# Performance work log

Measured on AMD Instinct MI355X. Metric: run time of the kernel, lower is better.

## Reference

```python
import jax, jax.numpy as jnp
import numpy as np


def setup_inputs() -> dict:
    key = jax.random.key(0)
    k1, k2, k3 = jax.random.split(key, 3)
    B, S, D_IN, D_OUT = 4, 2048, 4096, 4096
    x = jax.random.normal(k1, (B, S, D_IN), dtype=jnp.float32)
    weight = jax.random.normal(k2, (D_OUT, D_IN), dtype=jnp.float32) * 0.02
    bias = jax.random.normal(k3, (D_OUT,), dtype=jnp.float32) * 0.02
    return {"x": x, "weight": weight, "bias": bias}


def reference(x, weight, bias):
    # Column L1 norms over the output dim (torch.norm(w, p=1, dim=0)) -> [in_features]
    column_norms = jnp.abs(weight).sum(axis=0)
    q = jnp.quantile(column_norms, jnp.array([0.05, 0.95], dtype=column_norms.dtype))
    lower, upper = q[0], q[1]
    # NOTE: mask naming follows the source; 'outlier_columns' is actually the middle band.
    outlier_columns = (column_norms > lower) & (column_norms < upper)  # [in]
    binarized = ~outlier_columns  # columns that get rescaled (mask is inverted in source)

    # Row-wise abs-mean over the 'binarized' columns, detached. Shape [out, 1].
    n_bin = binarized.sum().astype(weight.dtype)
    scale = (jnp.abs(weight) * binarized[None, :]).sum(axis=-1, keepdims=True) / n_bin
    scale = jax.lax.stop_gradient(scale)

    # The STE sign assignment in the source is overwritten by w * scale, so the
    # effective binarized-column value is weight * scale (not sign(weight) * scale).
    w_bin = jnp.where(binarized[None, :], weight * scale, weight)  # [out, in]

    # F.linear(x, w_bin, bias)
    out = jnp.einsum('bsd,od->bso', x, w_bin) + bias
    return out
```

## Files before the change

### kernel.cpp

```cpp
#include <hip/hip_runtime.h>
#include <hip/hip_bf16.h>

typedef unsigned short u16;
typedef __bf16 bf16x8 __attribute__((ext_vector_type(8)));
typedef float f32x4 __attribute__((ext_vector_type(4)));
typedef __attribute__((address_space(1))) void* gp1_t;
typedef __attribute__((address_space(3))) void* lp3_t;

#define D_IN   4096
#define D_OUT  4096
#define M_ROWS 8192

#define OFF_NORMS  0u
#define OFF_QVALS  16384u
#define OFF_NBIN   16400u
#define OFF_MASK   16640u
#define OFF_SCALE  33024u
#define OFF_PART   49408u
#define OFF_XB     573696u
#define OFF_WB     67682560u

static __device__ __forceinline__ u16 f2bf(float f) {
    __hip_bfloat16 h = __float2bfloat16(f);
    u16 u; __builtin_memcpy(&u, &h, 2);
    return u;
}

__global__ void colnorm_partial(const float* __restrict__ W, float* __restrict__ part) {
    const int j  = blockIdx.x * 256 + threadIdx.x;
    const int r0 = blockIdx.y * 128;
    float s = 0.f;
    #pragma unroll 4
    for (int r = 0; r < 128; ++r) s += fabsf(W[(size_t)(r0 + r) * D_IN + j]);
    part[blockIdx.y * D_IN + j] = s;
}

__global__ void colnorm_reduce(const float* __restrict__ part, float* __restrict__ norms) {
    const int j = blockIdx.x * 256 + threadIdx.x;
    float s = 0.f;
    #pragma unroll
    for (int p = 0; p < 32; ++p) s += part[p * D_IN + j];
    norms[j] = s;
}

__global__ void rank_select(const float* __restrict__ norms, float* __restrict__ qvals) {
    __shared__ float sn[D_IN];
    const int tid = threadIdx.x;
    for (int i = tid; i < D_IN; i += 256) sn[i] = norms[i];
    __syncthreads();
    const int j = blockIdx.x * 256 + tid;
    const float vj = sn[j];
    int r = 0;
    #pragma unroll 8
    for (int i = 0; i < D_IN; ++i) {
        const float vi = sn[i];
        r += (vi < vj) || (vi == vj && i < j);
    }
    if      (r == 204)  qvals[0] = vj;
    else if (r == 205)  qvals[1] = vj;
    else if (r == 3890) qvals[2] = vj;
    else if (r == 3891) qvals[3] = vj;
}

__global__ void mask_count(const float* __restrict__ norms, const float* __restrict__ qvals,
                           float* __restrict__ mask, float* __restrict__ nbin) {
    __shared__ float wsum[16];
    const int tid = threadIdx.x;
    const float lower = qvals[0] + 0.75f * (qvals[1] - qvals[0]);
    const float upper = qvals[2] + 0.25f * (qvals[3] - qvals[2]);
    int cnt = 0;
    for (int i = tid; i < D_IN; i += 1024) {
        const float v = norms[i];
        const bool bin = !(v > lower && v < upper);
        mask[i] = bin ? 1.0f : 0.0f;
        cnt += bin ? 1 : 0;
    }
    #pragma unroll
    for (int off = 32; off > 0; off >>= 1) cnt += __shfl_down(cnt, off, 64);
    if ((tid & 63) == 0) wsum[tid >> 6] = (float)cnt;
    __syncthreads();
    if (tid == 0) {
        float s = 0.f;
        #pragma unroll
        for (int w = 0; w < 16; ++w) s += wsum[w];
        *nbin = s;
    }
}

__global__ void row_scale(const float* __restrict__ W, const float* __restrict__ mask,
                          const float* __restrict__ nbin, float* __restrict__ scale) {
    const int wave = threadIdx.x >> 6, lane = threadIdx.x & 63;
    const int o = blockIdx.x * 4 + wave;
    const float* row = W + (size_t)o * D_IN;
    float s = 0.f;
    #pragma unroll 4
    for (int j = lane; j < D_IN; j += 64) s += fabsf(row[j]) * mask[j];
    #pragma unroll
    for (int off = 32; off > 0; off >>= 1) s += __shfl_down(s, off, 64);
    if (lane == 0) scale[o] = s / *nbin;
}

__global__ void build_wbin(const float* __restrict__ W, const float* __restrict__ mask,
                           const float* __restrict__ scale, u16* __restrict__ wb) {
    const int o = blockIdx.x;
    const float sc = scale[o];
    const float4* row = (const float4*)(W + (size_t)o * D_IN);
    const float4* m4  = (const float4*)mask;
    ushort4* out = (ushort4*)(wb + (size_t)o * D_IN);
    #pragma unroll
    for (int it = 0; it < 4; ++it) {
        const int c = it * 256 + threadIdx.x;
        const float4 w = row[c];
        const float4 mm = m4[c];
        ushort4 r;
        r.x = f2bf(mm.x != 0.f ? w.x * sc : w.x);
        r.y = f2bf(mm.y != 0.f ? w.y * sc : w.y);
        r.z = f2bf(mm.z != 0.f ? w.z * sc : w.z);
        r.w = f2bf(mm.w != 0.f ? w.w * sc : w.w);
        out[c] = r;
    }
}

__global__ void cast_x(const float* __restrict__ x, u16* __restrict__ xb) {
    const size_t i4 = (size_t)blockIdx.x * 256 + threadIdx.x;
    const float4 v = ((const float4*)x)[i4];
    ushort4 r;
    r.x = f2bf(v.x); r.y = f2bf(v.y); r.z = f2bf(v.z); r.w = f2bf(v.w);
    ((ushort4*)xb)[i4] = r;
}

__global__ __launch_bounds__(256) void gemm_bt(const u16* __restrict__ A, const u16* __restrict__ B,
                                               const float* __restrict__ bias, float* __restrict__ C) {
    __shared__ u16 lA[128 * 32];
    __shared__ u16 lB[128 * 32];
    const int tid  = threadIdx.x;
    const int wave = tid >> 6, lane = tid & 63;
    const int wr = wave >> 1, wc = wave & 1;
    const int m0 = blockIdx.y * 128, n0 = blockIdx.x * 128;

    const int srow = tid >> 2;
    const int scol = (tid & 3) * 8;
    const u16* gA0 = A + (size_t)(m0 + srow) * D_IN + scol;
    const u16* gA1 = A + (size_t)(m0 + 64 + srow) * D_IN + scol;
    const u16* gB0 = B + (size_t)(n0 + srow) * D_IN + scol;
    const u16* gB1 = B + (size_t)(n0 + 64 + srow) * D_IN + scol;
    lp3_t lA0 = (lp3_t)(lA + wave * 512);
    lp3_t lA1 = (lp3_t)(lA + 2048 + wave * 512);
    lp3_t lB0 = (lp3_t)(lB + wave * 512);
    lp3_t lB1 = (lp3_t)(lB + 2048 + wave * 512);

    f32x4 acc[4][4] = {};

    const int koff = (lane >> 4) * 8;
    const int rsel = lane & 15;

    for (int kt = 0; kt < D_IN; kt += 32) {
        __builtin_amdgcn_global_load_lds((gp1_t)(gA0 + kt), lA0, 16, 0, 0);
        __builtin_amdgcn_global_load_lds((gp1_t)(gA1 + kt), lA1, 16, 0, 0);
        __builtin_amdgcn_global_load_lds((gp1_t)(gB0 + kt), lB0, 16, 0, 0);
        __builtin_amdgcn_global_load_lds((gp1_t)(gB1 + kt), lB1, 16, 0, 0);
        __syncthreads();

        bf16x8 af[4], bfv[4];
        #pragma unroll
        for (int mi = 0; mi < 4; ++mi)
            af[mi] = *(const bf16x8*)(lA + (wr * 64 + mi * 16 + rsel) * 32 + koff);
        #pragma unroll
        for (int ni = 0; ni < 4; ++ni)
            bfv[ni] = *(const bf16x8*)(lB + (wc * 64 + ni * 16 + rsel) * 32 + koff);
        #pragma unroll
        for (int mi = 0; mi < 4; ++mi)
            #pragma unroll
            for (int ni = 0; ni < 4; ++ni)
                acc[mi][ni] = __builtin_amdgcn_mfma_f32_16x16x32_bf16(af[mi], bfv[ni], acc[mi][ni], 0, 0, 0);
        __syncthreads();
    }

    const int cm = (lane >> 4) * 4;
    const int cn = lane & 15;
    #pragma unroll
    for (int ni = 0; ni < 4; ++ni) {
        const int n = n0 + wc * 64 + ni * 16 + cn;
        const float bv = bias[n];
        #pragma unroll
        for (int mi = 0; mi < 4; ++mi) {
            const int mbase = m0 + wr * 64 + mi * 16 + cm;
            #pragma unroll
            for (int r = 0; r < 4; ++r)
                C[(size_t)(mbase + r) * D_OUT + n] = acc[mi][ni][r] + bv;
        }
    }
}

extern "C" void kernel_launch(void* const* d_in, const int* in_sizes, int n_in,
                              void* d_out, int out_size, void* d_ws, size_t ws_size,
                              hipStream_t stream) {
    const float* x    = (const float*)d_in[0];
    const float* W    = (const float*)d_in[1];
    const float* bias = (const float*)d_in[2];
    float* out = (float*)d_out;

    char* ws = (char*)d_ws;
    float* norms = (float*)(ws + OFF_NORMS);
    float* qvals = (float*)(ws + OFF_QVALS);
    float* nbin  = (float*)(ws + OFF_NBIN);
    float* mask  = (float*)(ws + OFF_MASK);
    float* scale = (float*)(ws + OFF_SCALE);
    float* part  = (float*)(ws + OFF_PART);
    u16*   xb    = (u16*)(ws + OFF_XB);
    u16*   wb    = (u16*)(ws + OFF_WB);

    colnorm_partial<<<dim3(16, 32), 256, 0, stream>>>(W, part);
    colnorm_reduce<<<16, 256, 0, stream>>>(part, norms);
    rank_select<<<16, 256, 0, stream>>>(norms, qvals);
    mask_count<<<1, 1024, 0, stream>>>(norms, qvals, mask, nbin);
    row_scale<<<1024, 256, 0, stream>>>(W, mask, nbin, scale);
    build_wbin<<<4096, 256, 0, stream>>>(W, mask, scale, wb);
    cast_x<<<32768, 256, 0, stream>>>(x, xb);
    gemm_bt<<<dim3(D_OUT / 128, M_ROWS / 128), 256, 0, stream>>>(xb, wb, bias, out);
}
```

Measured before the change: 703.6 us.

## Fuse preprocessing kernels and swizzle GEMM LDS layout to avoid bank conflicts

Merges the column-norm partial/reduce kernels with the x-to-bf16 cast into one launch, using atomics into a zeroed norms buffer. Also merges mask/count, row-scale and weight-binarize into a single per-row kernel that keeps the row in registers. Separately, it XOR-rotates the 16-byte chunk placement in the GEMM's LDS tiles to cut bank conflicts on fragment reads. The atomic float accumulation makes the column norms order-nondeterministic, which could shift quantile ties slightly.

```diff
diff --git a/kernel.cpp b/kernel.cpp
--- a/kernel.cpp
+++ b/kernel.cpp
@@ -13,10 +13,6 @@
 
 #define OFF_NORMS  0u
 #define OFF_QVALS  16384u
-#define OFF_NBIN   16400u
-#define OFF_MASK   16640u
-#define OFF_SCALE  33024u
-#define OFF_PART   49408u
 #define OFF_XB     573696u
 #define OFF_WB     67682560u
 
@@ -26,21 +22,25 @@
     return u;
 }
 
-__global__ void colnorm_partial(const float* __restrict__ W, float* __restrict__ part) {
-    const int j  = blockIdx.x * 256 + threadIdx.x;
-    const int r0 = blockIdx.y * 128;
-    float s = 0.f;
-    #pragma unroll 4
-    for (int r = 0; r < 128; ++r) s += fabsf(W[(size_t)(r0 + r) * D_IN + j]);
-    part[blockIdx.y * D_IN + j] = s;
-}
-
-__global__ void colnorm_reduce(const float* __restrict__ part, float* __restrict__ norms) {
-    const int j = blockIdx.x * 256 + threadIdx.x;
-    float s = 0.f;
-    #pragma unroll
-    for (int p = 0; p < 32; ++p) s += part[p * D_IN + j];
-    norms[j] = s;
+__global__ __launch_bounds__(256) void k1_cast_colnorm(const float* __restrict__ x,
+                                                       const float* __restrict__ W,
+                                                       u16* __restrict__ xb,
+                                                       float* __restrict__ norms) {
+    const int b = blockIdx.x;
+    if (b < 512) {
+        const int j  = (b & 15) * 256 + threadIdx.x;
+        const int r0 = (b >> 4) * 128;
+        float s = 0.f;
+        #pragma unroll 4
+        for (int r = 0; r < 128; ++r) s += fabsf(W[(size_t)(r0 + r) * D_IN + j]);
+        atomicAdd(&norms[j], s);
+    } else {
+        const size_t i4 = (size_t)(b - 512) * 256 + threadIdx.x;
+        const float4 v = ((const float4*)x)[i4];
+        ushort4 r;
+        r.x = f2bf(v.x); r.y = f2bf(v.y); r.z = f2bf(v.z); r.w = f2bf(v.w);
+        ((ushort4*)xb)[i4] = r;
+    }
 }
 
 __global__ void rank_select(const float* __restrict__ norms, float* __restrict__ qvals) {
@@ -62,71 +62,58 @@
     else if (r == 3891) qvals[3] = vj;
 }
 
-__global__ void mask_count(const float* __restrict__ norms, const float* __restrict__ qvals,
-                           float* __restrict__ mask, float* __restrict__ nbin) {
-    __shared__ float wsum[16];
-    const int tid = threadIdx.x;
+__global__ __launch_bounds__(256) void k3_scale_wbin(const float* __restrict__ W,
+                                                     const float* __restrict__ norms,
+                                                     const float* __restrict__ qvals,
+                                                     u16* __restrict__ wb) {
+    __shared__ float red[8];
+    const int o = blockIdx.x, t = threadIdx.x;
+    const int wave = t >> 6, lane = t & 63;
     const float lower = qvals[0] + 0.75f * (qvals[1] - qvals[0]);
     const float upper = qvals[2] + 0.25f * (qvals[3] - qvals[2]);
-    int cnt = 0;
-    for (int i = tid; i < D_IN; i += 1024) {
-        const float v = norms[i];
-        const bool bin = !(v > lower && v < upper);
-        mask[i] = bin ? 1.0f : 0.0f;
-        cnt += bin ? 1 : 0;
-    }
-    #pragma unroll
-    for (int off = 32; off > 0; off >>= 1) cnt += __shfl_down(cnt, off, 64);
-    if ((tid & 63) == 0) wsum[tid >> 6] = (float)cnt;
+    const float4* row4 = (const float4*)(W + (size_t)o * D_IN);
+    const float4* n4   = (const float4*)norms;
+
+    float4 wv[4];
+    int binbits[4];
+    float cnt = 0.f, sum = 0.f;
+    #pragma unroll
+    for (int it = 0; it < 4; ++it) {
+        const int c = it * 256 + t;
+        wv[it] = row4[c];
+        const float4 nv = n4[c];
+        const bool b0 = !(nv.x > lower && nv.x < upper);
+        const bool b1 = !(nv.y > lower && nv.y < upper);
+        const bool b2 = !(nv.z > lower && nv.z < upper);
+        const bool b3 = !(nv.w > lower && nv.w < upper);
+        binbits[it] = (b0 ? 1 : 0) | (b1 ? 2 : 0) | (b2 ? 4 : 0) | (b3 ? 8 : 0);
+        cnt += (float)(b0 + b1 + b2 + b3);
+        sum += (b0 ? fabsf(wv[it].x) : 0.f) + (b1 ? fabsf(wv[it].y) : 0.f)
+             + (b2 ? fabsf(wv[it].z) : 0.f) + (b3 ? fabsf(wv[it].w) : 0.f);
+    }
+    #pragma unroll
+    for (int off = 32; off > 0; off >>= 1) {
+        cnt += __shfl_down(cnt, off, 64);
+        sum += __shfl_down(sum, off, 64);
+    }
+    if (lane == 0) { red[wave] = cnt; red[4 + wave] = sum; }
     __syncthreads();
-    if (tid == 0) {
-        float s = 0.f;
-        #pragma unroll
-        for (int w = 0; w < 16; ++w) s += wsum[w];
-        *nbin = s;
-    }
-}
-
-__global__ void row_scale(const float* __restrict__ W, const float* __restrict__ mask,
-                          const float* __restrict__ nbin, float* __restrict__ scale) {
-    const int wave = threadIdx.x >> 6, lane = threadIdx.x & 63;
-    const int o = blockIdx.x * 4 + wave;
-    const float* row = W + (size_t)o * D_IN;
-    float s = 0.f;
-    #pragma unroll 4
-    for (int j = lane; j < D_IN; j += 64) s += fabsf(row[j]) * mask[j];
-    #pragma unroll
-    for (int off = 32; off > 0; off >>= 1) s += __shfl_down(s, off, 64);
-    if (lane == 0) scale[o] = s / *nbin;
-}
-
-__global__ void build_wbin(const float* __restrict__ W, const float* __restrict__ mask,
-                           const float* __restrict__ scale, u16* __restrict__ wb) {
-    const int o = blockIdx.x;
-    const float sc = scale[o];
-    const float4* row = (const float4*)(W + (size_t)o * D_IN);
-    const float4* m4  = (const float4*)mask;
+    const float nbin = red[0] + red[1] + red[2] + red[3];
+    const float ssum = red[4] + red[5] + red[6] + red[7];
+    const float sc = ssum / nbin;
+
     ushort4* out = (ushort4*)(wb + (size_t)o * D_IN);
     #pragma unroll
     for (int it = 0; it < 4; ++it) {
-        const int c = it * 256 + threadIdx.x;
-        const float4 w = row[c];
-        const float4 mm = m4[c];
+        const int c = it * 256 + t;
+        const int bb = binbits[it];
         ushort4 r;
-        r.x = f2bf(mm.x != 0.f ? w.x * sc : w.x);
-        r.y = f2bf(mm.y != 0.f ? w.y * sc : w.y);
-        r.z = f2bf(mm.z != 0.f ? w.z * sc : w.z);
-        r.w = f2bf(mm.w != 0.f ? w.w * sc : w.w);
+        r.x = f2bf((bb & 1) ? wv[it].x * sc : wv[it].x);
+        r.y = f2bf((bb & 2) ? wv[it].y * sc : wv[it].y);
+        r.z = f2bf((bb & 4) ? wv[it].z * sc : wv[it].z);
+        r.w = f2bf((bb & 8) ? wv[it].w * sc : wv[it].w);
         out[c] = r;
     }
-}
-
-__global__ void cast_x(const float* __restrict__ x, u16* __restrict__ xb) {
-    const size_t i4 = (size_t)blockIdx.x * 256 + threadIdx.x;
-    const float4 v = ((const float4*)x)[i4];
-    ushort4 r;
-    r.x = f2bf(v.x); r.y = f2bf(v.y); r.z = f2bf(v.z); r.w = f2bf(v.w);
-    ((ushort4*)xb)[i4] = r;
 }
 
 __global__ __launch_bounds__(256) void gemm_bt(const u16* __restrict__ A, const u16* __restrict__ B,
@@ -138,12 +125,13 @@
     const int wr = wave >> 1, wc = wave & 1;
     const int m0 = blockIdx.y * 128, n0 = blockIdx.x * 128;
 
-    const int srow = tid >> 2;
-    const int scol = (tid & 3) * 8;
-    const u16* gA0 = A + (size_t)(m0 + srow) * D_IN + scol;
-    const u16* gA1 = A + (size_t)(m0 + 64 + srow) * D_IN + scol;
-    const u16* gB0 = B + (size_t)(n0 + srow) * D_IN + scol;
-    const u16* gB1 = B + (size_t)(n0 + 64 + srow) * D_IN + scol;
+    const int r    = tid >> 2;
+    const int cc   = ((tid & 3) - ((r >> 1) & 3)) & 3;
+    const int scol = cc * 8;
+    const u16* gA0 = A + (size_t)(m0 + r) * D_IN + scol;
+    const u16* gA1 = A + (size_t)(m0 + 64 + r) * D_IN + scol;
+    const u16* gB0 = B + (size_t)(n0 + r) * D_IN + scol;
+    const u16* gB1 = B + (size_t)(n0 + 64 + r) * D_IN + scol;
     lp3_t lA0 = (lp3_t)(lA + wave * 512);
     lp3_t lA1 = (lp3_t)(lA + 2048 + wave * 512);
     lp3_t lB0 = (lp3_t)(lB + wave * 512);
@@ -151,7 +139,7 @@
 
     f32x4 acc[4][4] = {};
 
-    const int koff = (lane >> 4) * 8;
+    const int cl   = lane >> 4;
     const int rsel = lane & 15;
 
     for (int kt = 0; kt < D_IN; kt += 32) {
@@ -163,11 +151,17 @@
 
         bf16x8 af[4], bfv[4];
         #pragma unroll
-        for (int mi = 0; mi < 4; ++mi)
-            af[mi] = *(const bf16x8*)(lA + (wr * 64 + mi * 16 + rsel) * 32 + koff);
-        #pragma unroll
-        for (int ni = 0; ni < 4; ++ni)
-            bfv[ni] = *(const bf16x8*)(lB + (wc * 64 + ni * 16 + rsel) * 32 + koff);
+        for (int mi = 0; mi < 4; ++mi) {
+            const int row = wr * 64 + mi * 16 + rsel;
+            const int s = row * 4 + ((cl + (row >> 1)) & 3);
+            af[mi] = *(const bf16x8*)(lA + s * 8);
+        }
+        #pragma unroll
+        for (int ni = 0; ni < 4; ++ni) {
+            const int row = wc * 64 + ni * 16 + rsel;
+            const int s = row * 4 + ((cl + (row >> 1)) & 3);
+            bfv[ni] = *(const bf16x8*)(lB + s * 8);
+        }
         #pragma unroll
         for (int mi = 0; mi < 4; ++mi)
             #pragma unroll
@@ -186,8 +180,8 @@
         for (int mi = 0; mi < 4; ++mi) {
             const int mbase = m0 + wr * 64 + mi * 16 + cm;
             #pragma unroll
-            for (int r = 0; r < 4; ++r)
-                C[(size_t)(mbase + r) * D_OUT + n] = acc[mi][ni][r] + bv;
+            for (int rr = 0; rr < 4; ++rr)
+                C[(size_t)(mbase + rr) * D_OUT + n] = acc[mi][ni][rr] + bv;
         }
     }
 }
@@ -203,19 +197,12 @@
     char* ws = (char*)d_ws;
     float* norms = (float*)(ws + OFF_NORMS);
     float* qvals = (float*)(ws + OFF_QVALS);
-    float* nbin  = (float*)(ws + OFF_NBIN);
-    float* mask  = (float*)(ws + OFF_MASK);
-    float* scale = (float*)(ws + OFF_SCALE);
-    float* part  = (float*)(ws + OFF_PART);
     u16*   xb    = (u16*)(ws + OFF_XB);
     u16*   wb    = (u16*)(ws + OFF_WB);
 
-    colnorm_partial<<<dim3(16, 32), 256, 0, stream>>>(W, part);
-    colnorm_reduce<<<16, 256, 0, stream>>>(part, norms);
+    hipMemsetAsync(norms, 0, D_IN * sizeof(float), stream);
+    k1_cast_colnorm<<<512 + 32768, 256, 0, stream>>>(x, W, xb, norms);
     rank_select<<<16, 256, 0, stream>>>(norms, qvals);
-    mask_count<<<1, 1024, 0, stream>>>(norms, qvals, mask, nbin);
-    row_scale<<<1024, 256, 0, stream>>>(W, mask, nbin, scale);
-    build_wbin<<<4096, 256, 0, stream>>>(W, mask, scale, wb);
-    cast_x<<<32768, 256, 0, stream>>>(x, xb);
+    k3_scale_wbin<<<4096, 256, 0, stream>>>(W, norms, qvals, wb);
     gemm_bt<<<dim3(D_OUT / 128, M_ROWS / 128), 256, 0, stream>>>(xb, wb, bias, out);
 }
```

Result: faster. 671.3 us (-4.6%).
